# Performance work log

Hardware: AMD Instinct MI355X
Metric: run time of the kernel (lower is better)

Reference implementation:

```python
import jax, jax.numpy as jnp
import numpy as np

N_NODES = 50000
N_EDGES = 800000
IN_DIM = 128
OUT_DIM = 128
NEG_INIT = -1e9  # matches torch fill_(-1e9) init for scatter amax
LEAKY_SLOPE = 0.01  # nn.LeakyReLU default


def setup_inputs() -> dict:
    key = jax.random.key(0)
    ks = jax.random.split(key, 8)
    x = jax.random.normal(ks[0], (N_NODES, IN_DIM), dtype=jnp.float32)
    edge_index = jax.random.randint(ks[1], (2, N_EDGES), 0, N_NODES, dtype=jnp.int64)
    edge_weight = jax.random.uniform(ks[2], (N_EDGES,), dtype=jnp.float32)
    # MLP params (nn.Linear default init: U(-1/sqrt(fan_in), 1/sqrt(fan_in)))
    s1 = 1.0 / np.sqrt(IN_DIM)
    s2 = 1.0 / np.sqrt(OUT_DIM)
    w1 = jax.random.uniform(ks[3], (OUT_DIM, IN_DIM), minval=-s1, maxval=s1, dtype=jnp.float32)
    b1 = jax.random.uniform(ks[4], (OUT_DIM,), minval=-s1, maxval=s1, dtype=jnp.float32)
    w2 = jax.random.uniform(ks[5], (OUT_DIM, OUT_DIM), minval=-s2, maxval=s2, dtype=jnp.float32)
    b2 = jax.random.uniform(ks[6], (OUT_DIM,), minval=-s2, maxval=s2, dtype=jnp.float32)
    eps = jnp.zeros((1,), dtype=jnp.float32)
    return {"x": x, "edge_index": edge_index, "edge_weight": edge_weight,
            "w1": w1, "b1": b1, "w2": w2, "b2": b2, "eps": eps}


def reference(x, edge_index, edge_weight, w1, b1, w2, b2, eps):
    src = edge_index[0]
    dst = edge_index[1]
    # gather + optional edge-weight scale: [E, D]
    messages = x[src] * edge_weight[:, None]
    # scatter-max to dst; init at -1e9 so include_self=False semantics hold
    agg = jnp.full(x.shape, NEG_INIT, dtype=x.dtype).at[dst].max(messages)
    agg = jnp.where(agg == NEG_INIT, jnp.zeros_like(agg), agg)  # isolated nodes -> 0
    h = (1.0 + eps) * x + agg  # eps broadcasts ([1])
    h = h @ w1.T + b1
    h = jnp.where(h >= 0, h, LEAKY_SLOPE * h)  # LeakyReLU
    out = h @ w2.T + b2
    return out
```

## Files before the change

kernel.cpp:

```cpp
#include <hip/hip_runtime.h>
#include <stdint.h>

#define NN 50000
#define NE 800000
#define D  128
#define NEG_INIT -1e9f
#define CAP 64
#define OVF_CAP 131072

#define FLAGS_OFF   0
#define CNT_OFF     64
#define OVF_CNT_OFF 50064
#define OVF_OFF     50068
#define BKT_OFF     312320
#define XBF_OFF     3512320
#define WBF_OFF     6712320

#define NBLK 196
#define HSTRIDE 136

typedef __attribute__((ext_vector_type(8))) short short8;
typedef __attribute__((ext_vector_type(4))) float float4v;

__device__ __forceinline__ float b2f(uint16_t u) {
    union { uint32_t u; float f; } v; v.u = ((uint32_t)u) << 16; return v.f;
}
__device__ __forceinline__ uint16_t f2b(float f) {
    union { float f; uint32_t u; } v; v.f = f;
    uint32_t r = v.u + 0x7fffu + ((v.u >> 16) & 1u);
    return (uint16_t)(r >> 16);
}

__global__ void probe_kernel(const uint16_t* __restrict__ xraw,
                             const int* __restrict__ eraw,
                             int* __restrict__ flags) {
    int t = threadIdx.x;
    float v0 = b2f(xraw[2 * t]);
    float v1 = b2f(xraw[2 * t + 1]);
    int bad = (!(v0 > -1e4f && v0 < 1e4f)) || (!(v1 > -1e4f && v1 < 1e4f));
    unsigned long long bm = __ballot(bad);
    int nz = (t < 32) ? (eraw[2 * t + 1] != 0) : 0;
    unsigned long long im = __ballot(nz);
    if (t == 0) { flags[0] = bm ? 1 : 0; flags[1] = im ? 0 : 1; }
}

__global__ __launch_bounds__(256) void prep_kernel(
    const uint16_t* __restrict__ xraw,
    const uint16_t* __restrict__ w1raw,
    const uint16_t* __restrict__ w2raw,
    int* __restrict__ ws)
{
    int bid = blockIdx.x;
    const int f32 = ws[0];
    if (bid < 6250) {
        int i4 = (bid * 256 + threadIdx.x) * 4;
        ushort* dst = (ushort*)(ws + XBF_OFF);
        if (f32) {
            float4 v = *(const float4*)((const float*)xraw + i4);
            ushort4 o; o.x = f2b(v.x); o.y = f2b(v.y); o.z = f2b(v.z); o.w = f2b(v.w);
            *(ushort4*)(dst + i4) = o;
        } else {
            *(ushort4*)(dst + i4) = *(const ushort4*)(xraw + i4);
        }
    } else if (bid < 6282) {
        int i4 = ((bid - 6250) * 256 + threadIdx.x) * 4;
        const uint16_t* src = (i4 < 16384) ? w1raw : w2raw;
        int off = i4 & 16383;
        ushort* dst = (ushort*)(ws + WBF_OFF);
        if (f32) {
            float4 v = *(const float4*)((const float*)src + off);
            ushort4 o; o.x = f2b(v.x); o.y = f2b(v.y); o.z = f2b(v.z); o.w = f2b(v.w);
            *(ushort4*)(dst + i4) = o;
        } else {
            *(ushort4*)(dst + i4) = *(const ushort4*)(src + off);
        }
    } else {
        int i = (bid - 6282) * 256 + threadIdx.x;
        if (i < NN) ws[CNT_OFF + i] = 0;
        if (i == 0)  ws[OVF_CNT_OFF] = 0;
    }
}

__global__ void fill_kernel(const int* __restrict__ eraw,
                            const uint16_t* __restrict__ ewraw,
                            int* __restrict__ ws) {
    int e = blockIdx.x * 256 + threadIdx.x;
    const int f32 = ws[0], i64 = ws[1];
    int src, dst;
    if (i64) {
        const long long* e64 = (const long long*)eraw;
        src = (int)e64[e];
        dst = (int)e64[NE + e];
    } else {
        src = eraw[e];
        dst = eraw[NE + e];
    }
    if ((unsigned)src >= NN || (unsigned)dst >= NN) return;
    uint w = f32 ? (uint)f2b(((const float*)ewraw)[e]) : (uint)ewraw[e];
    uint entry = (w << 16) | (uint)src;
    int slot = atomicAdd(ws + CNT_OFF + dst, 1);
    if (slot < CAP) {
        ((uint*)(ws + BKT_OFF))[(size_t)dst * CAP + slot] = entry;
    } else {
        int o = atomicAdd(ws + OVF_CNT_OFF, 1);
        if (o < OVF_CAP) {
            ws[OVF_OFF + 2 * o]     = dst;
            ws[OVF_OFF + 2 * o + 1] = (int)entry;
        }
    }
}

__global__ __launch_bounds__(256) void gmlp_kernel(
    const uint16_t* __restrict__ xraw,
    const uint16_t* __restrict__ b1raw,
    const uint16_t* __restrict__ b2raw,
    const uint16_t* __restrict__ epsraw,
    const int* __restrict__ ws,
    uint16_t* __restrict__ outraw)
{
    __shared__ uint   tl[16 * (HSTRIDE / 2)];
    __shared__ ushort hl[16 * HSTRIDE];

    const int tid  = threadIdx.x;
    const int wave = tid >> 6;
    const int lane = tid & 63;
    const int m    = lane & 15;
    const int quad = lane >> 4;
    const int node0 = blockIdx.x * 16;
    const int f32  = ws[0];

    const ushort* w1b = (const ushort*)(ws + WBF_OFF);
    const ushort* w2b = w1b + 16384;
    const uint*   xbf = (const uint*)(ws + XBF_OFF);
    const uint*   bkt = (const uint*)(ws + BKT_OFF);

    short8 bf1[2][4];
    float  bias1[2];
    #pragma unroll
    for (int t = 0; t < 2; ++t) {
        int ct = wave * 2 + t;
        const ushort* brow = w1b + (size_t)(ct * 16 + m) * 128 + quad * 8;
        #pragma unroll
        for (int kb = 0; kb < 4; ++kb) bf1[t][kb] = *(const short8*)(brow + kb * 32);
        bias1[t] = f32 ? ((const float*)b1raw)[ct * 16 + m] : b2f(b1raw[ct * 16 + m]);
    }
    const float eps1 = 1.0f + (f32 ? ((const float*)epsraw)[0] : b2f(epsraw[0]));

    for (int j = 0; j < 4; ++j) {
        int nl = wave * 4 + j;
        int n  = node0 + nl;
        int cnt_raw = ws[CNT_OFF + n];
        int cnt = (cnt_raw < CAP) ? cnt_raw : CAP;

        float m0[8], m1[8];
        #pragma unroll
        for (int u = 0; u < 8; ++u) { m0[u] = NEG_INIT; m1[u] = NEG_INIT; }

        const uint* brow = bkt + (size_t)n * CAP;
        for (int i = 0; i < cnt; i += 8) {
            #pragma unroll
            for (int u = 0; u < 8; ++u) {
                int idx  = i + u;
                int idxc = (idx < cnt - 1) ? idx : cnt - 1;
                uint e0  = brow[idxc];
                uint v   = xbf[(e0 & 0xffff) * 64 + lane];
                float w  = b2f((uint16_t)(e0 >> 16));
                float p0 = b2f((uint16_t)v) * w;
                float p1 = b2f((uint16_t)(v >> 16)) * w;
                bool ok  = idx < cnt;
                m0[u] = fmaxf(m0[u], ok ? p0 : NEG_INIT);
                m1[u] = fmaxf(m1[u], ok ? p1 : NEG_INIT);
            }
        }
        if (cnt_raw > CAP) {
            int novf = ws[OVF_CNT_OFF];
            if (novf > OVF_CAP) novf = OVF_CAP;
            for (int o = 0; o < novf; ++o) {
                if (ws[OVF_OFF + 2 * o] == n) {
                    uint e0 = (uint)ws[OVF_OFF + 2 * o + 1];
                    uint v  = xbf[(e0 & 0xffff) * 64 + lane];
                    float w = b2f((uint16_t)(e0 >> 16));
                    m0[0] = fmaxf(m0[0], b2f((uint16_t)v) * w);
                    m1[0] = fmaxf(m1[0], b2f((uint16_t)(v >> 16)) * w);
                }
            }
        }
        #pragma unroll
        for (int u = 4; u > 0; u >>= 1)
            #pragma unroll
            for (int v = 0; v < u; ++v) {
                m0[v] = fmaxf(m0[v], m0[v + u]);
                m1[v] = fmaxf(m1[v], m1[v + u]);
            }
        float mx = m0[0], my = m1[0];
        if (cnt_raw == 0) { mx = 0.f; my = 0.f; }

        float xs0, xs1;
        if (f32) {
            float2 v = ((const float2*)xraw)[(size_t)n * 64 + lane];
            xs0 = v.x; xs1 = v.y;
        } else {
            uint v = ((const uint*)xraw)[(size_t)n * 64 + lane];
            xs0 = b2f((uint16_t)v); xs1 = b2f((uint16_t)(v >> 16));
        }
        float t0 = eps1 * xs0 + mx;
        float t1 = eps1 * xs1 + my;
        tl[nl * (HSTRIDE / 2) + lane] = (uint)f2b(t0) | ((uint)f2b(t1) << 16);
    }
    __syncthreads();

    short8 a[4];
    {
        const ushort* arow = (const ushort*)tl + m * HSTRIDE + quad * 8;
        #pragma unroll
        for (int kb = 0; kb < 4; ++kb) a[kb] = *(const short8*)(arow + kb * 32);
    }

    #pragma unroll
    for (int t = 0; t < 2; ++t) {
        int ct = wave * 2 + t;
        float4v c = {0.f, 0.f, 0.f, 0.f};
        #pragma unroll
        for (int kb = 0; kb < 4; ++kb)
            c = __builtin_amdgcn_mfma_f32_16x16x32_bf16(a[kb], bf1[t][kb], c, 0, 0, 0);
        #pragma unroll
        for (int r = 0; r < 4; ++r) {
            float v = c[r] + bias1[t];
            v = (v >= 0.f) ? v : 0.01f * v;
            hl[(quad * 4 + r) * HSTRIDE + ct * 16 + m] = f2b(v);
        }
    }
    __syncthreads();

    short8 ah[4];
    {
        const ushort* hrow = hl + m * HSTRIDE + quad * 8;
        #pragma unroll
        for (int kb = 0; kb < 4; ++kb) ah[kb] = *(const short8*)(hrow + kb * 32);
    }

    #pragma unroll
    for (int t = 0; t < 2; ++t) {
        int ct = wave * 2 + t;
        float4v c = {0.f, 0.f, 0.f, 0.f};
        const ushort* brow = w2b + (size_t)(ct * 16 + m) * 128 + quad * 8;
        #pragma unroll
        for (int kb = 0; kb < 4; ++kb)
            c = __builtin_amdgcn_mfma_f32_16x16x32_bf16(ah[kb], *(const short8*)(brow + kb * 32), c, 0, 0, 0);
        float bias = f32 ? ((const float*)b2raw)[ct * 16 + m] : b2f(b2raw[ct * 16 + m]);
        #pragma unroll
        for (int r = 0; r < 4; ++r) {
            float v = c[r] + bias;
            size_t o = (size_t)(node0 + quad * 4 + r) * 128 + ct * 16 + m;
            if (f32) ((float*)outraw)[o] = v;
            else     outraw[o] = f2b(v);
        }
    }
}

extern "C" void kernel_launch(void* const* d_in, const int* in_sizes, int n_in,
                              void* d_out, int out_size, void* d_ws, size_t ws_size,
                              hipStream_t stream) {
    const uint16_t* x    = (const uint16_t*)d_in[0];
    const int*      eidx = (const int*)     d_in[1];
    const uint16_t* ew   = (const uint16_t*)d_in[2];
    const uint16_t* w1   = (const uint16_t*)d_in[3];
    const uint16_t* b1   = (const uint16_t*)d_in[4];
    const uint16_t* w2   = (const uint16_t*)d_in[5];
    const uint16_t* b2   = (const uint16_t*)d_in[6];
    const uint16_t* eps  = (const uint16_t*)d_in[7];
    uint16_t*       out  = (uint16_t*)d_out;
    int* ws = (int*)d_ws;

    probe_kernel<<<1, 64, 0, stream>>>(x, eidx, ws);
    prep_kernel<<<6250 + 32 + NBLK, 256, 0, stream>>>(x, w1, w2, ws);
    fill_kernel<<<NE / 256, 256, 0, stream>>>(eidx, ew, ws);
    gmlp_kernel<<<NN / 16, 256, 0, stream>>>(x, b1, b2, eps, ws, out);
}
```

Measured before the change: 216.9 us.

## Inline dtype probe into each kernel and widen gather unroll to 16

Removes the separate single-block probe kernel; each block of prep, fill and gmlp now re-derives the dtype flags from a few input elements into shared memory, which drops one launch and a global flag dependency. The gather loop now loads bucket entries as uint4 vectors and keeps 16 independent max accumulators instead of 8, to increase memory-level parallelism. W1 fragments and bias are loaded at their point of use instead of being hoisted, to reduce register pressure during the gather. The self term now reads the bf16 copy of x instead of raw x. The cost is a redundant probe and a barrier in every block, plus some rounding change when x is f32.

```diff
diff --git a/kernel.cpp b/kernel.cpp
--- a/kernel.cpp
+++ b/kernel.cpp
@@ -8,7 +8,6 @@
 #define CAP 64
 #define OVF_CAP 131072
 
-#define FLAGS_OFF   0
 #define CNT_OFF     64
 #define OVF_CNT_OFF 50064
 #define OVF_OFF     50068
@@ -31,27 +30,34 @@
     return (uint16_t)(r >> 16);
 }
 
-__global__ void probe_kernel(const uint16_t* __restrict__ xraw,
-                             const int* __restrict__ eraw,
-                             int* __restrict__ flags) {
+__device__ __forceinline__ void block_probe(const uint16_t* __restrict__ xraw,
+                                            const int* __restrict__ eraw,
+                                            int* sflags) {
     int t = threadIdx.x;
-    float v0 = b2f(xraw[2 * t]);
-    float v1 = b2f(xraw[2 * t + 1]);
-    int bad = (!(v0 > -1e4f && v0 < 1e4f)) || (!(v1 > -1e4f && v1 < 1e4f));
-    unsigned long long bm = __ballot(bad);
-    int nz = (t < 32) ? (eraw[2 * t + 1] != 0) : 0;
-    unsigned long long im = __ballot(nz);
-    if (t == 0) { flags[0] = bm ? 1 : 0; flags[1] = im ? 0 : 1; }
+    if (t < 64) {
+        float v0 = b2f(xraw[2 * t]);
+        float v1 = b2f(xraw[2 * t + 1]);
+        int bad = (!(v0 > -1e4f && v0 < 1e4f)) || (!(v1 > -1e4f && v1 < 1e4f));
+        unsigned long long bm = __ballot(bad);
+        int nz = (t < 32) ? (eraw[2 * t + 1] != 0) : 0;
+        unsigned long long im = __ballot(nz);
+        if (t == 0) { sflags[0] = bm ? 1 : 0; sflags[1] = im ? 0 : 1; }
+    }
+    __syncthreads();
 }
 
 __global__ __launch_bounds__(256) void prep_kernel(
     const uint16_t* __restrict__ xraw,
+    const int*      __restrict__ eraw,
     const uint16_t* __restrict__ w1raw,
     const uint16_t* __restrict__ w2raw,
     int* __restrict__ ws)
 {
+    __shared__ int sflags[2];
+    block_probe(xraw, eraw, sflags);
+    const int f32 = sflags[0];
+
     int bid = blockIdx.x;
-    const int f32 = ws[0];
     if (bid < 6250) {
         int i4 = (bid * 256 + threadIdx.x) * 4;
         ushort* dst = (ushort*)(ws + XBF_OFF);
@@ -81,11 +87,17 @@
     }
 }
 
-__global__ void fill_kernel(const int* __restrict__ eraw,
-                            const uint16_t* __restrict__ ewraw,
-                            int* __restrict__ ws) {
+__global__ __launch_bounds__(256) void fill_kernel(
+    const uint16_t* __restrict__ xraw,
+    const int*      __restrict__ eraw,
+    const uint16_t* __restrict__ ewraw,
+    int* __restrict__ ws)
+{
+    __shared__ int sflags[2];
+    block_probe(xraw, eraw, sflags);
+    const int f32 = sflags[0], i64 = sflags[1];
+
     int e = blockIdx.x * 256 + threadIdx.x;
-    const int f32 = ws[0], i64 = ws[1];
     int src, dst;
     if (i64) {
         const long long* e64 = (const long long*)eraw;
@@ -112,14 +124,19 @@
 
 __global__ __launch_bounds__(256) void gmlp_kernel(
     const uint16_t* __restrict__ xraw,
+    const int*      __restrict__ eraw,
     const uint16_t* __restrict__ b1raw,
     const uint16_t* __restrict__ b2raw,
     const uint16_t* __restrict__ epsraw,
     const int* __restrict__ ws,
     uint16_t* __restrict__ outraw)
 {
+    __shared__ int    sflags[2];
     __shared__ uint   tl[16 * (HSTRIDE / 2)];
     __shared__ ushort hl[16 * HSTRIDE];
+
+    block_probe(xraw, eraw, sflags);
+    const int f32 = sflags[0];
 
     const int tid  = threadIdx.x;
     const int wave = tid >> 6;
@@ -127,23 +144,12 @@
     const int m    = lane & 15;
     const int quad = lane >> 4;
     const int node0 = blockIdx.x * 16;
-    const int f32  = ws[0];
 
     const ushort* w1b = (const ushort*)(ws + WBF_OFF);
     const ushort* w2b = w1b + 16384;
     const uint*   xbf = (const uint*)(ws + XBF_OFF);
     const uint*   bkt = (const uint*)(ws + BKT_OFF);
 
-    short8 bf1[2][4];
-    float  bias1[2];
-    #pragma unroll
-    for (int t = 0; t < 2; ++t) {
-        int ct = wave * 2 + t;
-        const ushort* brow = w1b + (size_t)(ct * 16 + m) * 128 + quad * 8;
-        #pragma unroll
-        for (int kb = 0; kb < 4; ++kb) bf1[t][kb] = *(const short8*)(brow + kb * 32);
-        bias1[t] = f32 ? ((const float*)b1raw)[ct * 16 + m] : b2f(b1raw[ct * 16 + m]);
-    }
     const float eps1 = 1.0f + (f32 ? ((const float*)epsraw)[0] : b2f(epsraw[0]));
 
     for (int j = 0; j < 4; ++j) {
@@ -152,22 +158,24 @@
         int cnt_raw = ws[CNT_OFF + n];
         int cnt = (cnt_raw < CAP) ? cnt_raw : CAP;
 
-        float m0[8], m1[8];
-        #pragma unroll
-        for (int u = 0; u < 8; ++u) { m0[u] = NEG_INIT; m1[u] = NEG_INIT; }
+        float m0[16], m1[16];
+        #pragma unroll
+        for (int u = 0; u < 16; ++u) { m0[u] = NEG_INIT; m1[u] = NEG_INIT; }
 
         const uint* brow = bkt + (size_t)n * CAP;
-        for (int i = 0; i < cnt; i += 8) {
+        for (int i = 0; i < cnt; i += 16) {
+            uint4 q[4];
             #pragma unroll
-            for (int u = 0; u < 8; ++u) {
-                int idx  = i + u;
-                int idxc = (idx < cnt - 1) ? idx : cnt - 1;
-                uint e0  = brow[idxc];
-                uint v   = xbf[(e0 & 0xffff) * 64 + lane];
+            for (int qq = 0; qq < 4; ++qq) q[qq] = *(const uint4*)(brow + i + qq * 4);
+            #pragma unroll
+            for (int u = 0; u < 16; ++u) {
+                uint e0 = ((const uint*)q)[u];
+                bool ok = (i + u) < cnt;
+                uint idx = ok ? (e0 & 0xffffu) : 0u;
+                uint v = xbf[idx * 64 + lane];
                 float w  = b2f((uint16_t)(e0 >> 16));
                 float p0 = b2f((uint16_t)v) * w;
                 float p1 = b2f((uint16_t)(v >> 16)) * w;
-                bool ok  = idx < cnt;
                 m0[u] = fmaxf(m0[u], ok ? p0 : NEG_INIT);
                 m1[u] = fmaxf(m1[u], ok ? p1 : NEG_INIT);
             }
@@ -186,25 +194,18 @@
             }
         }
         #pragma unroll
-        for (int u = 4; u > 0; u >>= 1)
+        for (int u = 8; u > 0; u >>= 1)
             #pragma unroll
-            for (int v = 0; v < u; ++v) {
-                m0[v] = fmaxf(m0[v], m0[v + u]);
-                m1[v] = fmaxf(m1[v], m1[v + u]);
+            for (int v2 = 0; v2 < u; ++v2) {
+                m0[v2] = fmaxf(m0[v2], m0[v2 + u]);
+                m1[v2] = fmaxf(m1[v2], m1[v2 + u]);
             }
         float mx = m0[0], my = m1[0];
         if (cnt_raw == 0) { mx = 0.f; my = 0.f; }
 
-        float xs0, xs1;
-        if (f32) {
-            float2 v = ((const float2*)xraw)[(size_t)n * 64 + lane];
-            xs0 = v.x; xs1 = v.y;
-        } else {
-            uint v = ((const uint*)xraw)[(size_t)n * 64 + lane];
-            xs0 = b2f((uint16_t)v); xs1 = b2f((uint16_t)(v >> 16));
-        }
-        float t0 = eps1 * xs0 + mx;
-        float t1 = eps1 * xs1 + my;
+        uint xv = xbf[(size_t)n * 64 + lane];
+        float t0 = eps1 * b2f((uint16_t)xv) + mx;
+        float t1 = eps1 * b2f((uint16_t)(xv >> 16)) + my;
         tl[nl * (HSTRIDE / 2) + lane] = (uint)f2b(t0) | ((uint)f2b(t1) << 16);
     }
     __syncthreads();
@@ -220,12 +221,14 @@
     for (int t = 0; t < 2; ++t) {
         int ct = wave * 2 + t;
         float4v c = {0.f, 0.f, 0.f, 0.f};
+        const ushort* brow = w1b + (size_t)(ct * 16 + m) * 128 + quad * 8;
         #pragma unroll
         for (int kb = 0; kb < 4; ++kb)
-            c = __builtin_amdgcn_mfma_f32_16x16x32_bf16(a[kb], bf1[t][kb], c, 0, 0, 0);
+            c = __builtin_amdgcn_mfma_f32_16x16x32_bf16(a[kb], *(const short8*)(brow + kb * 32), c, 0, 0, 0);
+        float bias = f32 ? ((const float*)b1raw)[ct * 16 + m] : b2f(b1raw[ct * 16 + m]);
         #pragma unroll
         for (int r = 0; r < 4; ++r) {
-            float v = c[r] + bias1[t];
+            float v = c[r] + bias;
             v = (v >= 0.f) ? v : 0.01f * v;
             hl[(quad * 4 + r) * HSTRIDE + ct * 16 + m] = f2b(v);
         }
@@ -272,8 +275,7 @@
     uint16_t*       out  = (uint16_t*)d_out;
     int* ws = (int*)d_ws;
 
-    probe_kernel<<<1, 64, 0, stream>>>(x, eidx, ws);
-    prep_kernel<<<6250 + 32 + NBLK, 256, 0, stream>>>(x, w1, w2, ws);
-    fill_kernel<<<NE / 256, 256, 0, stream>>>(eidx, ew, ws);
-    gmlp_kernel<<<NN / 16, 256, 0, stream>>>(x, b1, b2, eps, ws, out);
-}
+    prep_kernel<<<6250 + 32 + NBLK, 256, 0, stream>>>(x, eidx, w1, w2, ws);
+    fill_kernel<<<NE / 256, 256, 0, stream>>>(x, eidx, ew, ws);
+    gmlp_kernel<<<NN / 16, 256, 0, stream>>>(x, eidx, b1, b2, eps, ws, out);
+}
```

Measured after the change: 209.8 us. 3.2% less time.
